# Optimization experiments

Measured on AMD Instinct MI355X. Metric: run time of the kernel, lower is better.

Reference implementation:

```python
import jax, jax.numpy as jnp
import numpy as np

EPS = 1e-12

def setup_inputs() -> dict:
    key = jax.random.key(0)
    k1, k2, k3 = jax.random.split(key, 3)
    B, D, N, NCLS = 1024, 512, 100000, 1000
    z = jax.random.normal(k1, (B, D), dtype=jnp.float32)
    lab_bank = jax.random.normal(k2, (N, D), dtype=jnp.float32)
    lab_labels = jax.random.randint(k3, (N,), 0, NCLS, dtype=jnp.int64)
    return {"z": z, "lab_bank": lab_bank, "lab_labels": lab_labels, "topk": 5}

def reference(z, lab_bank, lab_labels, topk):
    # cosine similarity: normalize query and bank, then GEMM
    zn = z / jnp.maximum(jnp.linalg.norm(z, axis=-1, keepdims=True), EPS)            # [B, D]
    bn = lab_bank / jnp.maximum(jnp.linalg.norm(lab_bank, axis=-1, keepdims=True), EPS)  # [N, D]
    sim = jnp.einsum('bd,nd->bn', zn, bn)                                            # [B, N]
    top_vals, top_idx = jax.lax.top_k(sim, topk)                                     # [B, k] each
    labels = lab_labels[top_idx]                                                     # [B, k]
    return top_idx, top_vals, labels
```

## Files before the change

### kernel.cpp

```cpp
#include <hip/hip_runtime.h>
#include <math.h>

#define DDIM 512
#define NS 96
#define KMASK 0xFFFFF800
#define NEG_INF (-3.0e38f)
#define IMAX 0x7fffffff

typedef _Float16 f16x8 __attribute__((ext_vector_type(8)));
typedef float    f32x4 __attribute__((ext_vector_type(4)));
typedef int      i32x4 __attribute__((ext_vector_type(4)));

__device__ __forceinline__ int imin(int a, int b) { return a < b ? a : b; }
__device__ __forceinline__ int imax(int a, int b) { return a > b ? a : b; }

__device__ __forceinline__ int med3(int a, int b, int c) {
    int d;
    asm("v_med3_i32 %0, %1, %2, %3" : "=v"(d) : "v"(a), "v"(b), "v"(c));
    return d;
}

__device__ __forceinline__ void glds16(const void* g, void* l) {
    __builtin_amdgcn_global_load_lds((const __attribute__((address_space(1))) void*)g,
                                     (__attribute__((address_space(3))) void*)l, 16, 0, 0);
}

#define KBAR() do { asm volatile("s_waitcnt vmcnt(0)" ::: "memory"); \
                    __builtin_amdgcn_s_barrier();                    \
                    asm volatile("" ::: "memory"); } while (0)

__global__ __launch_bounds__(256) void split_tile_k(
    const float* __restrict__ zsrc, const float* __restrict__ bsrc,
    unsigned* __restrict__ ztile, unsigned* __restrict__ btile,
    float* __restrict__ rz, float* __restrict__ rb,
    int zrows, int brows, int nbBlocks) {

    const int bx = blockIdx.x;
    const float* src; unsigned* tile; float* rn; int rows; int blk;
    if (bx < nbBlocks) { src = bsrc; tile = btile; rn = rb; rows = brows; blk = bx; }
    else               { src = zsrc; tile = ztile; rn = rz; rows = zrows; blk = bx - nbBlocks; }

    const int t = threadIdx.x;
    const int r = t >> 1, hf = t & 1;
    const int R = blk * 128 + r;
    const bool valid = R < rows;
    const float* srow = src + (size_t)(valid ? R : 0) * DDIM + hf * 16;

    float ss = 0.f;
    for (int ks = 0; ks < 16; ++ks) {
        float4 v0 = *(const float4*)(srow + ks * 32);
        float4 v1 = *(const float4*)(srow + ks * 32 + 4);
        float4 v2 = *(const float4*)(srow + ks * 32 + 8);
        float4 v3 = *(const float4*)(srow + ks * 32 + 12);
        ss += v0.x*v0.x + v0.y*v0.y + v0.z*v0.z + v0.w*v0.w
            + v1.x*v1.x + v1.y*v1.y + v1.z*v1.z + v1.w*v1.w
            + v2.x*v2.x + v2.y*v2.y + v2.z*v2.z + v2.w*v2.w
            + v3.x*v3.x + v3.y*v3.y + v3.z*v3.z + v3.w*v3.w;
    }
    ss += __shfl_xor(ss, 1, 64);
    const float scale = valid ? 1.0f / fmaxf(sqrtf(ss), 1e-12f) : 0.0f;
    if (hf == 0) rn[R] = scale;

    for (int ks = 0; ks < 16; ++ks) {
        float4 v0 = *(const float4*)(srow + ks * 32);
        float4 v1 = *(const float4*)(srow + ks * 32 + 4);
        float4 v2 = *(const float4*)(srow + ks * 32 + 8);
        float4 v3 = *(const float4*)(srow + ks * 32 + 12);
        unsigned o[8];
        o[0] = __builtin_bit_cast(unsigned, __builtin_amdgcn_cvt_pkrtz(v0.x*scale, v0.y*scale));
        o[1] = __builtin_bit_cast(unsigned, __builtin_amdgcn_cvt_pkrtz(v0.z*scale, v0.w*scale));
        o[2] = __builtin_bit_cast(unsigned, __builtin_amdgcn_cvt_pkrtz(v1.x*scale, v1.y*scale));
        o[3] = __builtin_bit_cast(unsigned, __builtin_amdgcn_cvt_pkrtz(v1.z*scale, v1.w*scale));
        o[4] = __builtin_bit_cast(unsigned, __builtin_amdgcn_cvt_pkrtz(v2.x*scale, v2.y*scale));
        o[5] = __builtin_bit_cast(unsigned, __builtin_amdgcn_cvt_pkrtz(v2.z*scale, v2.w*scale));
        o[6] = __builtin_bit_cast(unsigned, __builtin_amdgcn_cvt_pkrtz(v3.x*scale, v3.y*scale));
        o[7] = __builtin_bit_cast(unsigned, __builtin_amdgcn_cvt_pkrtz(v3.z*scale, v3.w*scale));
        unsigned* dst = tile + ((size_t)(blk * 16 + ks) * 128 + r) * 16 + hf * 8;
        *(i32x4*)dst       = *(i32x4*)o;
        *(i32x4*)(dst + 4) = *(i32x4*)(o + 4);
    }
}

__global__ __launch_bounds__(256, 4) void gemm_screen_k(
    const unsigned* __restrict__ zh, const unsigned* __restrict__ bh,
    int* __restrict__ cand, int N, int nChunks) {

    __shared__ alignas(16) int smem[8192];

    const int t = threadIdx.x;
    const int w = t >> 6, lane = t & 63;
    const int wz = w >> 1, wb = w & 1;
    const int quad = lane >> 4, l16 = lane & 15;
    const int split = blockIdx.x, rowblk = blockIdx.y;
    const int soff = w * 1024 + lane * 16;

    int T[4][4];
    #pragma unroll
    for (int zi = 0; zi < 4; ++zi)
        #pragma unroll
        for (int q = 0; q < 4; ++q) T[zi][q] = (int)0x80000000;

    {
        const char* gA = (const char*)zh + (size_t)(rowblk * 16) * 8192;
        const char* gB = (const char*)bh + (size_t)(split * 16) * 8192;
        glds16(gA + soff,        (char*)smem + soff);
        glds16(gA + 4096 + soff, (char*)smem + 4096 + soff);
        glds16(gB + soff,        (char*)smem + 8192 + soff);
        glds16(gB + 4096 + soff, (char*)smem + 12288 + soff);
    }

    int iter = 0;
    for (int chunk = split; chunk < nChunks; chunk += NS, ++iter) {
        f32x4 acc[4][4];
        #pragma unroll
        for (int bi = 0; bi < 4; ++bi)
            #pragma unroll
            for (int zi = 0; zi < 4; ++zi) acc[bi][zi] = (f32x4){0.f, 0.f, 0.f, 0.f};

        #pragma unroll 2
        for (int ks = 0; ks < 16; ++ks) {
            KBAR();
            if (ks < 15) {
                const char* gA = (const char*)zh + (size_t)(rowblk * 16 + ks + 1) * 8192;
                const char* gB = (const char*)bh + (size_t)(chunk * 16 + ks + 1) * 8192;
                char* l = (char*)smem + (((ks & 1) ^ 1) << 14);
                glds16(gA + soff,        l + soff);
                glds16(gA + 4096 + soff, l + 4096 + soff);
                glds16(gB + soff,        l + 8192 + soff);
                glds16(gB + 4096 + soff, l + 12288 + soff);
            } else if (chunk + NS < nChunks) {
                const char* gA = (const char*)zh + (size_t)(rowblk * 16) * 8192;
                const char* gB = (const char*)bh + (size_t)((chunk + NS) * 16) * 8192;
                glds16(gA + soff,        (char*)smem + soff);
                glds16(gA + 4096 + soff, (char*)smem + 4096 + soff);
                glds16(gB + soff,        (char*)smem + 8192 + soff);
                glds16(gB + 4096 + soff, (char*)smem + 12288 + soff);
            }

            const unsigned short* A  = (const unsigned short*)((const char*)smem + ((ks & 1) << 14));
            const unsigned short* Bb = (const unsigned short*)((const char*)smem + ((ks & 1) << 14) + 8192);
            f16x8 af[4], bf[4];
            #pragma unroll
            for (int zi = 0; zi < 4; ++zi)
                af[zi] = __builtin_bit_cast(f16x8,
                    *(const i32x4*)(A + (wz * 64 + zi * 16 + l16) * 32 + quad * 8));
            #pragma unroll
            for (int bi = 0; bi < 4; ++bi)
                bf[bi] = __builtin_bit_cast(f16x8,
                    *(const i32x4*)(Bb + (wb * 64 + bi * 16 + l16) * 32 + quad * 8));
            #pragma unroll
            for (int bi = 0; bi < 4; ++bi)
                #pragma unroll
                for (int zi = 0; zi < 4; ++zi)
                    acc[bi][zi] = __builtin_amdgcn_mfma_f32_16x16x32_f16(bf[bi], af[zi], acc[bi][zi], 0, 0, 0);
        }

        const int tbase = (iter << 7) | (wb << 6) | (quad << 2);
        #pragma unroll
        for (int zi = 0; zi < 4; ++zi)
            #pragma unroll
            for (int bi = 0; bi < 4; ++bi)
                #pragma unroll
                for (int rr = 0; rr < 4; ++rr) {
                    int kk = (__float_as_int(acc[bi][zi][rr]) & KMASK) | (tbase + bi * 16 + rr);
                    int n1 = med3(kk, T[zi][0], T[zi][1]);
                    int n2 = med3(kk, T[zi][1], T[zi][2]);
                    int n3 = med3(kk, T[zi][2], T[zi][3]);
                    T[zi][0] = imax(kk, T[zi][0]);
                    T[zi][1] = n1; T[zi][2] = n2; T[zi][3] = n3;
                }
    }

    #pragma unroll
    for (int zi = 0; zi < 4; ++zi) {
        int a0 = T[zi][0], a1 = T[zi][1], a2 = T[zi][2], a3 = T[zi][3];
        #pragma unroll
        for (int off = 16; off <= 32; off <<= 1) {
            int p0 = __shfl_xor(a0, off, 64);
            int p1 = __shfl_xor(a1, off, 64);
            int p2 = __shfl_xor(a2, off, 64);
            int p3 = __shfl_xor(a3, off, 64);
            int m0 = imax(a0, p3), m1 = imax(a1, p2), m2 = imax(a2, p1), m3 = imax(a3, p0);
            int b0 = imax(m0, m2), b2 = imin(m0, m2), b1 = imax(m1, m3), b3 = imin(m1, m3);
            a0 = imax(b0, b1); a1 = imin(b0, b1); a2 = imax(b2, b3); a3 = imin(b2, b3);
        }
        if (quad == 0) {
            i32x4 outk = { a0, a1, a2, a3 };
            const int row = rowblk * 128 + wz * 64 + zi * 16 + l16;
            *(i32x4*)(cand + (((size_t)row * NS + split) * 2 + wb) * 4) = outk;
        }
    }
}

__global__ __launch_bounds__(256) void merge_rescore_k(
    const int* __restrict__ cand,
    const float* __restrict__ z, const float* __restrict__ bank,
    const float* __restrict__ rz, const float* __restrict__ rb,
    const int* __restrict__ labels, float* __restrict__ out, int BK, int N) {

    __shared__ float zrow[DDIM];
    __shared__ int   idxs[32];
    __shared__ float dots[32];

    const int row = blockIdx.x;
    const int t = threadIdx.x, w = t >> 6, lane = t & 63;

    {   float2 v = *(const float2*)(z + (size_t)row * DDIM + t * 2);
        zrow[t * 2] = v.x; zrow[t * 2 + 1] = v.y; }

    if (w == 0) {
        int k[12];
        const int* cp = cand + (size_t)row * (NS * 2 * 4) + lane * 12;
        #pragma unroll
        for (int q = 0; q < 12; ++q) k[q] = cp[q];
        for (int r = 0; r < 32; ++r) {
            int lk = k[0], lq = 0;
            #pragma unroll
            for (int q = 1; q < 12; ++q) if (k[q] > lk) { lk = k[q]; lq = q; }
            int wk = lk, wl = lane, wq = lq;
            #pragma unroll
            for (int off = 32; off > 0; off >>= 1) {
                int ok = __shfl_xor(wk, off, 64);
                int ol = __shfl_xor(wl, off, 64);
                int oq = __shfl_xor(wq, off, 64);
                if (ok > wk || (ok == wk && ol < wl)) { wk = ok; wl = ol; wq = oq; }
            }
            if (lane == wl) {
                #pragma unroll
                for (int q = 0; q < 12; ++q) if (q == wq) k[q] = (int)0x80000000;
            }
            if (lane == 0) {
                int j = wl * 12 + wq;
                int split = j >> 3;
                int c = wk & 127, it = (wk >> 7) & 15;
                int gi = (it * NS + split) * 128 + c;
                idxs[r] = gi < N ? gi : 0;
            }
        }
    }
    __syncthreads();

    #pragma unroll
    for (int jj = 0; jj < 8; ++jj) {
        const int ci = idxs[w * 8 + jj];
        const float* br = bank + (size_t)ci * DDIM + lane * 8;
        float4 x0 = *(const float4*)br;
        float4 x1 = *(const float4*)(br + 4);
        const float* zz = zrow + lane * 8;
        float4 z0 = *(const float4*)zz;
        float4 z1 = *(const float4*)(zz + 4);
        float s = x0.x*z0.x + x0.y*z0.y + x0.z*z0.z + x0.w*z0.w
                + x1.x*z1.x + x1.y*z1.y + x1.z*z1.z + x1.w*z1.w;
        #pragma unroll
        for (int off = 32; off > 0; off >>= 1) s += __shfl_xor(s, off, 64);
        if (lane == 0) dots[w * 8 + jj] = s;
    }
    __syncthreads();

    if (w == 0) {
        const float rzv = rz[row];
        float v; int ii;
        if (lane < 32) { ii = idxs[lane]; v = dots[lane] * rzv * rb[ii]; }
        else           { ii = IMAX;       v = NEG_INF; }
        for (int r = 0; r < 5; ++r) {
            float bv = v; int bi = ii;
            #pragma unroll
            for (int off = 32; off > 0; off >>= 1) {
                float ov = __shfl_xor(bv, off, 64);
                int   oi = __shfl_xor(bi, off, 64);
                if (ov > bv || (ov == bv && oi < bi)) { bv = ov; bi = oi; }
            }
            if (v == bv && ii == bi) { v = NEG_INF; ii = IMAX; }
            if (lane == 0) {
                out[(size_t)row * 5 + r]          = (float)bi;
                out[BK + (size_t)row * 5 + r]     = bv;
                out[2 * BK + (size_t)row * 5 + r] = (float)labels[bi];
            }
        }
    }
}

extern "C" void kernel_launch(void* const* d_in, const int* in_sizes, int n_in,
                              void* d_out, int out_size, void* d_ws, size_t ws_size,
                              hipStream_t stream) {
    const float* z    = (const float*)d_in[0];
    const float* bank = (const float*)d_in[1];
    const int*   lab  = (const int*)d_in[2];
    const int B = in_sizes[0] / DDIM;
    const int N = in_sizes[1] / DDIM;
    const int BK = out_size / 3;
    const int nChunks = (N + 127) >> 7;
    float* out = (float*)d_out;
    char* ws = (char*)d_ws;

    const size_t o_rz = 0;
    const size_t o_rb = 4096;
    const size_t o_zh = o_rb + (size_t)nChunks * 128 * 4;
    const size_t o_bh = o_zh + (size_t)(B / 128) * 16 * 8192;
    const size_t o_cv = o_bh + (size_t)nChunks * 16 * 8192;

    float* rz = (float*)(ws + o_rz);
    float* rb = (float*)(ws + o_rb);
    unsigned* zh = (unsigned*)(ws + o_zh);
    unsigned* bh = (unsigned*)(ws + o_bh);
    int* cand = (int*)(ws + o_cv);

    split_tile_k<<<nChunks + B / 128, 256, 0, stream>>>(z, bank, zh, bh, rz, rb, B, N, nChunks);
    gemm_screen_k<<<dim3(NS, B / 128), 256, 0, stream>>>(zh, bh, cand, N, nChunks);
    merge_rescore_k<<<B, 256, 0, stream>>>(cand, z, bank, rz, rb, lab, out, BK, N);
}
```

Before: 489.8 us.

## Convert bank to fp16 in one pass and apply row norms in the GEMM epilogue

The split/tile kernel now converts unnormalized rows to fp16 in the same pass that computes the sum of squares, so each input row is read once instead of twice. The per-row inverse norm is instead multiplied into the GEMM accumulators before top-k screening, which needs a small load of the rb norms per chunk. The fp16 tile layout is also changed to a quad-major arrangement, and the LDS fragment reads are updated to match, which likely alters bank-conflict behaviour. Risks: fp16 conversion of unnormalized values loses relative precision and could overflow for large-magnitude rows, and query rows are no longer scaled, which is harmless for ranking.

```diff
diff --git a/kernel.cpp b/kernel.cpp
--- a/kernel.cpp
+++ b/kernel.cpp
@@ -56,33 +56,31 @@
             + v1.x*v1.x + v1.y*v1.y + v1.z*v1.z + v1.w*v1.w
             + v2.x*v2.x + v2.y*v2.y + v2.z*v2.z + v2.w*v2.w
             + v3.x*v3.x + v3.y*v3.y + v3.z*v3.z + v3.w*v3.w;
+        unsigned o[8];
+        o[0] = __builtin_bit_cast(unsigned, __builtin_amdgcn_cvt_pkrtz(v0.x, v0.y));
+        o[1] = __builtin_bit_cast(unsigned, __builtin_amdgcn_cvt_pkrtz(v0.z, v0.w));
+        o[2] = __builtin_bit_cast(unsigned, __builtin_amdgcn_cvt_pkrtz(v1.x, v1.y));
+        o[3] = __builtin_bit_cast(unsigned, __builtin_amdgcn_cvt_pkrtz(v1.z, v1.w));
+        o[4] = __builtin_bit_cast(unsigned, __builtin_amdgcn_cvt_pkrtz(v2.x, v2.y));
+        o[5] = __builtin_bit_cast(unsigned, __builtin_amdgcn_cvt_pkrtz(v2.z, v2.w));
+        o[6] = __builtin_bit_cast(unsigned, __builtin_amdgcn_cvt_pkrtz(v3.x, v3.y));
+        o[7] = __builtin_bit_cast(unsigned, __builtin_amdgcn_cvt_pkrtz(v3.z, v3.w));
+        if (!valid) {
+            #pragma unroll
+            for (int q = 0; q < 8; ++q) o[q] = 0u;
+        }
+        unsigned* dst = tile + (size_t)(blk * 16 + ks) * 2048
+                             + (r >> 4) * 256 + (hf * 32 + (r & 15)) * 4;
+        *(i32x4*)dst        = *(i32x4*)o;
+        *(i32x4*)(dst + 64) = *(i32x4*)(o + 4);
     }
     ss += __shfl_xor(ss, 1, 64);
-    const float scale = valid ? 1.0f / fmaxf(sqrtf(ss), 1e-12f) : 0.0f;
-    if (hf == 0) rn[R] = scale;
-
-    for (int ks = 0; ks < 16; ++ks) {
-        float4 v0 = *(const float4*)(srow + ks * 32);
-        float4 v1 = *(const float4*)(srow + ks * 32 + 4);
-        float4 v2 = *(const float4*)(srow + ks * 32 + 8);
-        float4 v3 = *(const float4*)(srow + ks * 32 + 12);
-        unsigned o[8];
-        o[0] = __builtin_bit_cast(unsigned, __builtin_amdgcn_cvt_pkrtz(v0.x*scale, v0.y*scale));
-        o[1] = __builtin_bit_cast(unsigned, __builtin_amdgcn_cvt_pkrtz(v0.z*scale, v0.w*scale));
-        o[2] = __builtin_bit_cast(unsigned, __builtin_amdgcn_cvt_pkrtz(v1.x*scale, v1.y*scale));
-        o[3] = __builtin_bit_cast(unsigned, __builtin_amdgcn_cvt_pkrtz(v1.z*scale, v1.w*scale));
-        o[4] = __builtin_bit_cast(unsigned, __builtin_amdgcn_cvt_pkrtz(v2.x*scale, v2.y*scale));
-        o[5] = __builtin_bit_cast(unsigned, __builtin_amdgcn_cvt_pkrtz(v2.z*scale, v2.w*scale));
-        o[6] = __builtin_bit_cast(unsigned, __builtin_amdgcn_cvt_pkrtz(v3.x*scale, v3.y*scale));
-        o[7] = __builtin_bit_cast(unsigned, __builtin_amdgcn_cvt_pkrtz(v3.z*scale, v3.w*scale));
-        unsigned* dst = tile + ((size_t)(blk * 16 + ks) * 128 + r) * 16 + hf * 8;
-        *(i32x4*)dst       = *(i32x4*)o;
-        *(i32x4*)(dst + 4) = *(i32x4*)(o + 4);
-    }
+    if (hf == 0) rn[R] = valid ? 1.0f / fmaxf(sqrtf(ss), 1e-12f) : 0.0f;
 }
 
 __global__ __launch_bounds__(256, 4) void gemm_screen_k(
     const unsigned* __restrict__ zh, const unsigned* __restrict__ bh,
+    const float* __restrict__ rb,
     int* __restrict__ cand, int N, int nChunks) {
 
     __shared__ alignas(16) int smem[8192];
@@ -116,6 +114,7 @@
         for (int bi = 0; bi < 4; ++bi)
             #pragma unroll
             for (int zi = 0; zi < 4; ++zi) acc[bi][zi] = (f32x4){0.f, 0.f, 0.f, 0.f};
+        f32x4 rbv[4];
 
         #pragma unroll 2
         for (int ks = 0; ks < 16; ++ks) {
@@ -136,18 +135,23 @@
                 glds16(gB + soff,        (char*)smem + 8192 + soff);
                 glds16(gB + 4096 + soff, (char*)smem + 12288 + soff);
             }
-
-            const unsigned short* A  = (const unsigned short*)((const char*)smem + ((ks & 1) << 14));
-            const unsigned short* Bb = (const unsigned short*)((const char*)smem + ((ks & 1) << 14) + 8192);
+            if (ks == 0) {
+                #pragma unroll
+                for (int bi = 0; bi < 4; ++bi)
+                    rbv[bi] = *(const f32x4*)(rb + chunk * 128 + wb * 64 + bi * 16 + quad * 4);
+            }
+
+            const char* Ab = (const char*)smem + ((ks & 1) << 14);
+            const char* Bb = Ab + 8192;
             f16x8 af[4], bf[4];
             #pragma unroll
             for (int zi = 0; zi < 4; ++zi)
                 af[zi] = __builtin_bit_cast(f16x8,
-                    *(const i32x4*)(A + (wz * 64 + zi * 16 + l16) * 32 + quad * 8));
+                    *(const i32x4*)(Ab + (wz * 4 + zi) * 1024 + quad * 256 + l16 * 16));
             #pragma unroll
             for (int bi = 0; bi < 4; ++bi)
                 bf[bi] = __builtin_bit_cast(f16x8,
-                    *(const i32x4*)(Bb + (wb * 64 + bi * 16 + l16) * 32 + quad * 8));
+                    *(const i32x4*)(Bb + (wb * 4 + bi) * 1024 + quad * 256 + l16 * 16));
             #pragma unroll
             for (int bi = 0; bi < 4; ++bi)
                 #pragma unroll
@@ -162,7 +166,8 @@
             for (int bi = 0; bi < 4; ++bi)
                 #pragma unroll
                 for (int rr = 0; rr < 4; ++rr) {
-                    int kk = (__float_as_int(acc[bi][zi][rr]) & KMASK) | (tbase + bi * 16 + rr);
+                    float v = acc[bi][zi][rr] * rbv[bi][rr];
+                    int kk = (__float_as_int(v) & KMASK) | (tbase + bi * 16 + rr);
                     int n1 = med3(kk, T[zi][0], T[zi][1]);
                     int n2 = med3(kk, T[zi][1], T[zi][2]);
                     int n3 = med3(kk, T[zi][2], T[zi][3]);
@@ -306,6 +311,6 @@
     int* cand = (int*)(ws + o_cv);
 
     split_tile_k<<<nChunks + B / 128, 256, 0, stream>>>(z, bank, zh, bh, rz, rb, B, N, nChunks);
-    gemm_screen_k<<<dim3(NS, B / 128), 256, 0, stream>>>(zh, bh, cand, N, nChunks);
+    gemm_screen_k<<<dim3(NS, B / 128), 256, 0, stream>>>(zh, bh, rb, cand, N, nChunks);
     merge_rescore_k<<<B, 256, 0, stream>>>(cand, z, bank, rz, rb, lab, out, BK, N);
 }
```

After: 469.6 us. -4.1%, faster.
